# Kernel optimization log

Hardware: AMD Instinct MI355X
Metric: run time of the kernel (lower is better)

The kernel has to match this reference:

```python
import jax, jax.numpy as jnp
import numpy as np

LN_EPS = 1e-5
N, D = 512, 512


def setup_inputs() -> dict:
    key = jax.random.key(0)
    ks = jax.random.split(key, 3)
    s1 = 1.0 / np.sqrt(2 * D)  # torch Linear default-ish scale
    s2 = 1.0 / np.sqrt(D)
    return {
        "embeddings": jax.random.normal(ks[0], (N, D), jnp.float32),
        "W1": jax.random.normal(ks[1], (2 * D, D), jnp.float32) * s1,  # [in, out]
        "b1": jnp.zeros((D,), jnp.float32),
        "gamma": jnp.ones((D,), jnp.float32),
        "beta": jnp.zeros((D,), jnp.float32),
        "W2": jax.random.normal(ks[2], (D, 1), jnp.float32) * s2,
        "b2": jnp.zeros((1,), jnp.float32),
    }


def reference(embeddings, W1, b1, gamma, beta, W2, b2):
    d = embeddings.shape[-1]
    # Linear(2D -> D) on cat(e_i, e_j) decomposes into two GEMMs + broadcast add,
    # avoiding materializing the [N, N, 2D] concatenated pair tensor.
    left = embeddings @ W1[:d]              # [N, D]  (contribution of e_i)
    right = embeddings @ W1[d:] + b1        # [N, D]  (contribution of e_j + bias)
    h = left[:, None, :] + right[None, :, :]  # [N, N, D]
    # LayerNorm over last dim (eps matches torch default)
    mu = h.mean(axis=-1, keepdims=True)
    var = ((h - mu) ** 2).mean(axis=-1, keepdims=True)
    h = (h - mu) * jax.lax.rsqrt(var + LN_EPS) * gamma + beta
    # exact GELU (torch nn.GELU default)
    h = jax.nn.gelu(h, approximate=False)
    s = jax.nn.sigmoid(jnp.squeeze(h @ W2, -1) + b2[0])  # [N, N]
    # original loop only evaluates pairs i <= j and mirrors to (j, i)
    n = s.shape[0]
    upper = jnp.arange(n)[:, None] <= jnp.arange(n)[None, :]
    return jnp.where(upper, s, s.T)
```

## Files before the change

kernel.cpp:

```cpp
#include <hip/hip_runtime.h>


#define N_ 512
#define D_ 512

__global__ __launch_bounds__(256) void k_gemm(const float* __restrict__ E,
                                              const float* __restrict__ W1,
                                              const float* __restrict__ b1,
                                              float* __restrict__ W ) {
    __shared__ float e[16][516];
    const int t = threadIdx.x;
    const int cc = (blockIdx.x & 7) * 128;
    const int r0 = (blockIdx.x >> 3) * 16;
    const int half = cc >> 9;
    const int c = (cc & 511) + (t & 31) * 4;
    const int rp = (t >> 5) * 2;

    for (int x = t; x < 16 * 128; x += 256) {
        int r = x >> 7, c4 = (x & 127) << 2;
        *(float4*)&e[r][c4] = *(const float4*)&E[(r0 + r) * D_ + c4];
    }
    __syncthreads();

    const float* __restrict__ wp = W1 + (half << 18) + c;
    float4 a0 = {0.f, 0.f, 0.f, 0.f}, a1 = {0.f, 0.f, 0.f, 0.f};
#pragma unroll 4
    for (int k = 0; k < D_; k += 4) {
        float4 e0 = *(float4*)&e[rp][k];
        float4 e1 = *(float4*)&e[rp + 1][k];
        float4 wa = *(const float4*)(wp + ((k + 0) << 9));
        float4 wb = *(const float4*)(wp + ((k + 1) << 9));
        float4 wc = *(const float4*)(wp + ((k + 2) << 9));
        float4 wd = *(const float4*)(wp + ((k + 3) << 9));
        a0.x = fmaf(e0.x, wa.x, a0.x); a0.y = fmaf(e0.x, wa.y, a0.y);
        a0.z = fmaf(e0.x, wa.z, a0.z); a0.w = fmaf(e0.x, wa.w, a0.w);
        a1.x = fmaf(e1.x, wa.x, a1.x); a1.y = fmaf(e1.x, wa.y, a1.y);
        a1.z = fmaf(e1.x, wa.z, a1.z); a1.w = fmaf(e1.x, wa.w, a1.w);
        a0.x = fmaf(e0.y, wb.x, a0.x); a0.y = fmaf(e0.y, wb.y, a0.y);
        a0.z = fmaf(e0.y, wb.z, a0.z); a0.w = fmaf(e0.y, wb.w, a0.w);
        a1.x = fmaf(e1.y, wb.x, a1.x); a1.y = fmaf(e1.y, wb.y, a1.y);
        a1.z = fmaf(e1.y, wb.z, a1.z); a1.w = fmaf(e1.y, wb.w, a1.w);
        a0.x = fmaf(e0.z, wc.x, a0.x); a0.y = fmaf(e0.z, wc.y, a0.y);
        a0.z = fmaf(e0.z, wc.z, a0.z); a0.w = fmaf(e0.z, wc.w, a0.w);
        a1.x = fmaf(e1.z, wc.x, a1.x); a1.y = fmaf(e1.z, wc.y, a1.y);
        a1.z = fmaf(e1.z, wc.z, a1.z); a1.w = fmaf(e1.z, wc.w, a1.w);
        a0.x = fmaf(e0.w, wd.x, a0.x); a0.y = fmaf(e0.w, wd.y, a0.y);
        a0.z = fmaf(e0.w, wd.z, a0.z); a0.w = fmaf(e0.w, wd.w, a0.w);
        a1.x = fmaf(e1.w, wd.x, a1.x); a1.y = fmaf(e1.w, wd.y, a1.y);
        a1.z = fmaf(e1.w, wd.z, a1.z); a1.w = fmaf(e1.w, wd.w, a1.w);
    }
    if (half) {
        float4 bb = *(const float4*)(b1 + c);
        a0.x += bb.x; a0.y += bb.y; a0.z += bb.z; a0.w += bb.w;
        a1.x += bb.x; a1.y += bb.y; a1.z += bb.z; a1.w += bb.w;
    }
    *(float4*)(W + ((half << 9) + r0 + rp) * D_ + c) = a0;
    *(float4*)(W + ((half << 9) + r0 + rp + 1) * D_ + c) = a1;
}

__device__ __forceinline__ float block_sum(float v, float* sred, int t) {
#pragma unroll
    for (int off = 32; off > 0; off >>= 1) v += __shfl_xor(v, off, 64);
    int wave = t >> 6;
    if ((t & 63) == 0) sred[wave] = v;
    __syncthreads();
    float s = sred[0] + sred[1] + sred[2] + sred[3];
    __syncthreads();
    return s;
}

__global__ __launch_bounds__(256) void k_center(float* __restrict__ W,
                                                float* __restrict__ var) {
    __shared__ float sred[4];
    const int r = blockIdx.x, t = threadIdx.x;
    float* p = W + r * D_;
    float v0 = p[t], v1 = p[t + 256];
    float s = block_sum(v0 + v1, sred, t);
    float mean = s * (1.f / D_);
    float c0 = v0 - mean, c1 = v1 - mean;
    float ss = block_sum(c0 * c0 + c1 * c1, sred, t);
    p[t] = c0;
    p[t + 256] = c1;
    if (t == 0) var[r] = ss * (1.f / D_);
}

__device__ __forceinline__ void gelu_acc(float l, float r, float g, float be,
                                         float w, float rstd, float& acc) {
    float s = l + r;
    float x = fmaf(s * rstd, g, be);
    float x2 = x * x;
    float q = x * fmaf(-0.10294340f, x2, -2.30220935f);
    float eq = __builtin_amdgcn_exp2f(q);
    float ge = x * __builtin_amdgcn_rcpf(1.f + eq);
    acc = fmaf(ge, w, acc);
}

__global__ __launch_bounds__(256) void k_pair(const float* __restrict__ W,
                                              const float* __restrict__ var,
                                              const float* __restrict__ gf,
                                              const float* __restrict__ bef,
                                              const float* __restrict__ wf,
                                              const float* __restrict__ b2f,
                                              float* __restrict__ out) {
    __shared__ float ls[16][260];
    __shared__ float rs[16][260];
    __shared__ float red[4096];
    __shared__ float rstd_s[256];

    const int b = blockIdx.x;
    int I = (int)((65.0f - sqrtf(4225.0f - 8.0f * (float)b)) * 0.5f);
    if (I < 0) I = 0;
    if (I > 31) I = 31;
#define S_(i) (32 * (i) - ((i) * ((i)-1)) / 2)
    while (S_(I) > b) --I;
    while (S_(I + 1) <= b) ++I;
    const int J = I + (b - S_(I));
#undef S_

    const int t = threadIdx.x;
    const int ks = t & 15, pt = t >> 4;
    const int i4 = (pt & 3) * 4, j4 = (pt >> 2) * 4;
    const int Ibase = I * 16, Jbase = N_ + J * 16;

    float cv[16];
#pragma unroll
    for (int c = 0; c < 16; ++c) cv[c] = 0.f;
    for (int kb = 0; kb < D_; kb += 256) {
        for (int x = t; x < 16 * 64; x += 256) {
            int r = x >> 6, c4 = (x & 63) << 2;
            *(float4*)&ls[r][c4] = *(const float4*)&W[(Ibase + r) * D_ + kb + c4];
            *(float4*)&rs[r][c4] = *(const float4*)&W[(Jbase + r) * D_ + kb + c4];
        }
        __syncthreads();
#pragma unroll
        for (int it = 0; it < 4; ++it) {
            const int kq = (it * 16 + ks) * 4;
            float4 lq[4], rq[4];
#pragma unroll
            for (int d = 0; d < 4; ++d) {
                lq[d] = *(float4*)&ls[i4 + d][kq];
                rq[d] = *(float4*)&rs[j4 + d][kq];
            }
#pragma unroll
            for (int di = 0; di < 4; ++di)
#pragma unroll
                for (int dj = 0; dj < 4; ++dj)
                    cv[di * 4 + dj] += lq[di].x * rq[dj].x + lq[di].y * rq[dj].y +
                                       lq[di].z * rq[dj].z + lq[di].w * rq[dj].w;
        }
        __syncthreads();
    }
#pragma unroll
    for (int c = 0; c < 16; ++c) red[ks * 256 + pt * 16 + c] = cv[c];
    __syncthreads();

    const int ri = t >> 4, rj = t & 15;
    const int rpt = (ri >> 2) + ((rj >> 2) << 2);
    const int rc = (ri & 3) * 4 + (rj & 3);
    {
        float cov = 0.f;
#pragma unroll
        for (int k2 = 0; k2 < 16; ++k2) cov += red[k2 * 256 + rpt * 16 + rc];
        float varh = var[Ibase + ri] + var[Jbase + rj] + cov * (2.f / D_) + 1e-5f;
        rstd_s[t] = rsqrtf(varh);
    }
    __syncthreads();

    float rst[16];
#pragma unroll
    for (int di = 0; di < 4; ++di)
#pragma unroll
        for (int dj = 0; dj < 4; ++dj)
            rst[di * 4 + dj] = rstd_s[(i4 + di) * 16 + (j4 + dj)];
    float ac[16];
#pragma unroll
    for (int c = 0; c < 16; ++c) ac[c] = 0.f;
    for (int kb = 0; kb < D_; kb += 256) {
        for (int x = t; x < 16 * 64; x += 256) {
            int r = x >> 6, c4 = (x & 63) << 2;
            *(float4*)&ls[r][c4] = *(const float4*)&W[(Ibase + r) * D_ + kb + c4];
            *(float4*)&rs[r][c4] = *(const float4*)&W[(Jbase + r) * D_ + kb + c4];
        }
        __syncthreads();
#pragma unroll
        for (int it = 0; it < 4; ++it) {
            const int kq = (it * 16 + ks) * 4;
            float4 g4 = *(const float4*)&gf[kb + kq];
            float4 be4 = *(const float4*)&bef[kb + kq];
            float4 w4 = *(const float4*)&wf[kb + kq];
            float4 lq[4], rq[4];
#pragma unroll
            for (int d = 0; d < 4; ++d) {
                lq[d] = *(float4*)&ls[i4 + d][kq];
                rq[d] = *(float4*)&rs[j4 + d][kq];
            }
#pragma unroll
            for (int di = 0; di < 4; ++di)
#pragma unroll
                for (int dj = 0; dj < 4; ++dj) {
                    float rr = rst[di * 4 + dj];
                    float& a = ac[di * 4 + dj];
                    gelu_acc(lq[di].x, rq[dj].x, g4.x, be4.x, w4.x, rr, a);
                    gelu_acc(lq[di].y, rq[dj].y, g4.y, be4.y, w4.y, rr, a);
                    gelu_acc(lq[di].z, rq[dj].z, g4.z, be4.z, w4.z, rr, a);
                    gelu_acc(lq[di].w, rq[dj].w, g4.w, be4.w, w4.w, rr, a);
                }
        }
        __syncthreads();
    }
#pragma unroll
    for (int c = 0; c < 16; ++c) red[ks * 256 + pt * 16 + c] = ac[c];
    __syncthreads();

    {
        float z = b2f[0];
#pragma unroll
        for (int k2 = 0; k2 < 16; ++k2) z += red[k2 * 256 + rpt * 16 + rc];
        float sg = __builtin_amdgcn_rcpf(1.f + __builtin_amdgcn_exp2f(-1.44269504f * z));
        const int gi = Ibase + ri, gj = (Jbase - N_) + rj;
        if (gi <= gj) {
            out[gi * N_ + gj] = sg;
            out[gj * N_ + gi] = sg;
        }
    }
}

extern "C" void kernel_launch(void* const* d_in, const int* in_sizes, int n_in,
                              void* d_out, int out_size, void* d_ws, size_t ws_size,
                              hipStream_t stream) {
    const float* E     = (const float*)d_in[0];
    const float* W1    = (const float*)d_in[1];
    const float* b1    = (const float*)d_in[2];
    const float* gamma = (const float*)d_in[3];
    const float* beta  = (const float*)d_in[4];
    const float* w2    = (const float*)d_in[5];
    const float* b2    = (const float*)d_in[6];
    float* out = (float*)d_out;

    float* F    = (float*)d_ws;
    float* lcrc = F;
    float* var  = F + 1024 * 512;

    k_gemm<<<256, 256, 0, stream>>>(E, W1, b1, lcrc);
    k_center<<<1024, 256, 0, stream>>>(lcrc, var);
    k_pair<<<528, 256, 0, stream>>>(lcrc, var, gamma, beta, w2, b2, out);
}
```

Baseline: 132.0 us.

## Shrink pair-kernel shared memory for occupancy and split GEMM into smaller tiles

The pair kernel now stages W in 128-column chunks with padded rows and aliases the reduction buffer onto the staging area, cutting shared memory from about 50KB to about 17KB. It also adds a min-blocks hint of 4 to launch_bounds so more blocks can be resident per CU. The k-slice mapping is rearranged so each wave owns separate k-slices, and the reduction layout is transposed with padding to avoid bank conflicts. The GEMM kernel uses 64-column tiles with one row per thread and launches twice as many blocks, which halves register accumulators but re-reads weights more often.

After: 171.3 us. 29.8% more time.

```diff
diff --git a/kernel.cpp b/kernel.cpp
--- a/kernel.cpp
+++ b/kernel.cpp
@@ -8,54 +8,43 @@
                                               const float* __restrict__ W1,
                                               const float* __restrict__ b1,
                                               float* __restrict__ W ) {
-    __shared__ float e[16][516];
+    __shared__ float e[16 * 516];
     const int t = threadIdx.x;
-    const int cc = (blockIdx.x & 7) * 128;
-    const int r0 = (blockIdx.x >> 3) * 16;
+    const int cc = (blockIdx.x & 15) * 64;
+    const int r0 = (blockIdx.x >> 4) * 16;
     const int half = cc >> 9;
-    const int c = (cc & 511) + (t & 31) * 4;
-    const int rp = (t >> 5) * 2;
+    const int c = (cc & 511) + (t & 15) * 4;
+    const int r = t >> 4;
 
     for (int x = t; x < 16 * 128; x += 256) {
-        int r = x >> 7, c4 = (x & 127) << 2;
-        *(float4*)&e[r][c4] = *(const float4*)&E[(r0 + r) * D_ + c4];
+        int rr = x >> 7, q = x & 127;
+        *(float4*)&e[rr * 516 + q * 4] = *(const float4*)&E[(r0 + rr) * D_ + q * 4];
     }
     __syncthreads();
 
     const float* __restrict__ wp = W1 + (half << 18) + c;
-    float4 a0 = {0.f, 0.f, 0.f, 0.f}, a1 = {0.f, 0.f, 0.f, 0.f};
+    float4 acc = {0.f, 0.f, 0.f, 0.f};
 #pragma unroll 4
     for (int k = 0; k < D_; k += 4) {
-        float4 e0 = *(float4*)&e[rp][k];
-        float4 e1 = *(float4*)&e[rp + 1][k];
+        float4 e4 = *(float4*)&e[r * 516 + k];
         float4 wa = *(const float4*)(wp + ((k + 0) << 9));
         float4 wb = *(const float4*)(wp + ((k + 1) << 9));
         float4 wc = *(const float4*)(wp + ((k + 2) << 9));
         float4 wd = *(const float4*)(wp + ((k + 3) << 9));
-        a0.x = fmaf(e0.x, wa.x, a0.x); a0.y = fmaf(e0.x, wa.y, a0.y);
-        a0.z = fmaf(e0.x, wa.z, a0.z); a0.w = fmaf(e0.x, wa.w, a0.w);
-        a1.x = fmaf(e1.x, wa.x, a1.x); a1.y = fmaf(e1.x, wa.y, a1.y);
-        a1.z = fmaf(e1.x, wa.z, a1.z); a1.w = fmaf(e1.x, wa.w, a1.w);
-        a0.x = fmaf(e0.y, wb.x, a0.x); a0.y = fmaf(e0.y, wb.y, a0.y);
-        a0.z = fmaf(e0.y, wb.z, a0.z); a0.w = fmaf(e0.y, wb.w, a0.w);
-        a1.x = fmaf(e1.y, wb.x, a1.x); a1.y = fmaf(e1.y, wb.y, a1.y);
-        a1.z = fmaf(e1.y, wb.z, a1.z); a1.w = fmaf(e1.y, wb.w, a1.w);
-        a0.x = fmaf(e0.z, wc.x, a0.x); a0.y = fmaf(e0.z, wc.y, a0.y);
-        a0.z = fmaf(e0.z, wc.z, a0.z); a0.w = fmaf(e0.z, wc.w, a0.w);
-        a1.x = fmaf(e1.z, wc.x, a1.x); a1.y = fmaf(e1.z, wc.y, a1.y);
-        a1.z = fmaf(e1.z, wc.z, a1.z); a1.w = fmaf(e1.z, wc.w, a1.w);
-        a0.x = fmaf(e0.w, wd.x, a0.x); a0.y = fmaf(e0.w, wd.y, a0.y);
-        a0.z = fmaf(e0.w, wd.z, a0.z); a0.w = fmaf(e0.w, wd.w, a0.w);
-        a1.x = fmaf(e1.w, wd.x, a1.x); a1.y = fmaf(e1.w, wd.y, a1.y);
-        a1.z = fmaf(e1.w, wd.z, a1.z); a1.w = fmaf(e1.w, wd.w, a1.w);
+        acc.x = fmaf(e4.x, wa.x, acc.x); acc.y = fmaf(e4.x, wa.y, acc.y);
+        acc.z = fmaf(e4.x, wa.z, acc.z); acc.w = fmaf(e4.x, wa.w, acc.w);
+        acc.x = fmaf(e4.y, wb.x, acc.x); acc.y = fmaf(e4.y, wb.y, acc.y);
+        acc.z = fmaf(e4.y, wb.z, acc.z); acc.w = fmaf(e4.y, wb.w, acc.w);
+        acc.x = fmaf(e4.z, wc.x, acc.x); acc.y = fmaf(e4.z, wc.y, acc.y);
+        acc.z = fmaf(e4.z, wc.z, acc.z); acc.w = fmaf(e4.z, wc.w, acc.w);
+        acc.x = fmaf(e4.w, wd.x, acc.x); acc.y = fmaf(e4.w, wd.y, acc.y);
+        acc.z = fmaf(e4.w, wd.z, acc.z); acc.w = fmaf(e4.w, wd.w, acc.w);
     }
     if (half) {
         float4 bb = *(const float4*)(b1 + c);
-        a0.x += bb.x; a0.y += bb.y; a0.z += bb.z; a0.w += bb.w;
-        a1.x += bb.x; a1.y += bb.y; a1.z += bb.z; a1.w += bb.w;
-    }
-    *(float4*)(W + ((half << 9) + r0 + rp) * D_ + c) = a0;
-    *(float4*)(W + ((half << 9) + r0 + rp + 1) * D_ + c) = a1;
+        acc.x += bb.x; acc.y += bb.y; acc.z += bb.z; acc.w += bb.w;
+    }
+    *(float4*)(W + ((half << 9) + r0 + r) * D_ + c) = acc;
 }
 
 __device__ __forceinline__ float block_sum(float v, float* sred, int t) {
@@ -95,17 +84,18 @@
     acc = fmaf(ge, w, acc);
 }
 
-__global__ __launch_bounds__(256) void k_pair(const float* __restrict__ W,
-                                              const float* __restrict__ var,
-                                              const float* __restrict__ gf,
-                                              const float* __restrict__ bef,
-                                              const float* __restrict__ wf,
-                                              const float* __restrict__ b2f,
-                                              float* __restrict__ out) {
-    __shared__ float ls[16][260];
-    __shared__ float rs[16][260];
-    __shared__ float red[4096];
-    __shared__ float rstd_s[256];
+__global__ __launch_bounds__(256, 4) void k_pair(const float* __restrict__ W,
+                                                 const float* __restrict__ var,
+                                                 const float* __restrict__ gf,
+                                                 const float* __restrict__ bef,
+                                                 const float* __restrict__ wf,
+                                                 const float* __restrict__ b2f,
+                                                 float* __restrict__ out) {
+    __shared__ float smem[4416];
+    float* ls = smem;
+    float* rs = smem + 2080;
+    float* red = smem;
+    float* rstd_s = smem + 4160;
 
     const int b = blockIdx.x;
     int I = (int)((65.0f - sqrtf(4225.0f - 8.0f * (float)b)) * 0.5f);
@@ -118,28 +108,33 @@
 #undef S_
 
     const int t = threadIdx.x;
-    const int ks = t & 15, pt = t >> 4;
-    const int i4 = (pt & 3) * 4, j4 = (pt >> 2) * 4;
+    const int l = t & 63, wv = t >> 6;
+    const int pt = l & 15, s = l >> 4;
+    const int pi = pt & 3, pj = pt >> 2;
+    const int sigma = wv * 4 + s;
+    const int i4 = pi * 4, j4 = pj * 4;
     const int Ibase = I * 16, Jbase = N_ + J * 16;
 
     float cv[16];
 #pragma unroll
     for (int c = 0; c < 16; ++c) cv[c] = 0.f;
-    for (int kb = 0; kb < D_; kb += 256) {
-        for (int x = t; x < 16 * 64; x += 256) {
-            int r = x >> 6, c4 = (x & 63) << 2;
-            *(float4*)&ls[r][c4] = *(const float4*)&W[(Ibase + r) * D_ + kb + c4];
-            *(float4*)&rs[r][c4] = *(const float4*)&W[(Jbase + r) * D_ + kb + c4];
-        }
-        __syncthreads();
-#pragma unroll
-        for (int it = 0; it < 4; ++it) {
-            const int kq = (it * 16 + ks) * 4;
+    for (int c = 0; c < 4; ++c) {
+#pragma unroll
+        for (int it = 0; it < 2; ++it) {
+            int x = t + it * 256;
+            int rr = x >> 5, q = x & 31;
+            *(float4*)&ls[rr * 130 + q * 4] = *(const float4*)&W[(Ibase + rr) * D_ + c * 128 + q * 4];
+            *(float4*)&rs[rr * 130 + q * 4] = *(const float4*)&W[(Jbase + rr) * D_ + c * 128 + q * 4];
+        }
+        __syncthreads();
+#pragma unroll
+        for (int mm = 0; mm < 2; ++mm) {
+            const int off = 64 * mm + 4 * sigma;
             float4 lq[4], rq[4];
 #pragma unroll
             for (int d = 0; d < 4; ++d) {
-                lq[d] = *(float4*)&ls[i4 + d][kq];
-                rq[d] = *(float4*)&rs[j4 + d][kq];
+                lq[d] = *(float4*)&ls[(i4 + d) * 130 + off];
+                rq[d] = *(float4*)&rs[(j4 + d) * 130 + off];
             }
 #pragma unroll
             for (int di = 0; di < 4; ++di)
@@ -151,17 +146,18 @@
         __syncthreads();
     }
 #pragma unroll
-    for (int c = 0; c < 16; ++c) red[ks * 256 + pt * 16 + c] = cv[c];
-    __syncthreads();
-
-    const int ri = t >> 4, rj = t & 15;
-    const int rpt = (ri >> 2) + ((rj >> 2) << 2);
-    const int rc = (ri & 3) * 4 + (rj & 3);
+    for (int di = 0; di < 4; ++di)
+#pragma unroll
+        for (int dj = 0; dj < 4; ++dj)
+            red[sigma * 257 + (j4 + dj) * 16 + i4 + di] = cv[di * 4 + dj];
+    __syncthreads();
+
     {
-        float cov = 0.f;
-#pragma unroll
-        for (int k2 = 0; k2 < 16; ++k2) cov += red[k2 * 256 + rpt * 16 + rc];
-        float varh = var[Ibase + ri] + var[Jbase + rj] + cov * (2.f / D_) + 1e-5f;
+        const int ii = t & 15, jj = t >> 4;
+        float covsum = 0.f;
+#pragma unroll
+        for (int ss = 0; ss < 16; ++ss) covsum += red[ss * 257 + t];
+        float varh = var[Ibase + ii] + var[Jbase + jj] + covsum * (2.f / D_) + 1e-5f;
         rstd_s[t] = rsqrtf(varh);
     }
     __syncthreads();
@@ -171,53 +167,60 @@
     for (int di = 0; di < 4; ++di)
 #pragma unroll
         for (int dj = 0; dj < 4; ++dj)
-            rst[di * 4 + dj] = rstd_s[(i4 + di) * 16 + (j4 + dj)];
+            rst[di * 4 + dj] = rstd_s[(j4 + dj) * 16 + i4 + di];
     float ac[16];
 #pragma unroll
     for (int c = 0; c < 16; ++c) ac[c] = 0.f;
-    for (int kb = 0; kb < D_; kb += 256) {
-        for (int x = t; x < 16 * 64; x += 256) {
-            int r = x >> 6, c4 = (x & 63) << 2;
-            *(float4*)&ls[r][c4] = *(const float4*)&W[(Ibase + r) * D_ + kb + c4];
-            *(float4*)&rs[r][c4] = *(const float4*)&W[(Jbase + r) * D_ + kb + c4];
-        }
-        __syncthreads();
-#pragma unroll
-        for (int it = 0; it < 4; ++it) {
-            const int kq = (it * 16 + ks) * 4;
-            float4 g4 = *(const float4*)&gf[kb + kq];
-            float4 be4 = *(const float4*)&bef[kb + kq];
-            float4 w4 = *(const float4*)&wf[kb + kq];
+    for (int c = 0; c < 4; ++c) {
+#pragma unroll
+        for (int it = 0; it < 2; ++it) {
+            int x = t + it * 256;
+            int rr = x >> 5, q = x & 31;
+            *(float4*)&ls[rr * 130 + q * 4] = *(const float4*)&W[(Ibase + rr) * D_ + c * 128 + q * 4];
+            *(float4*)&rs[rr * 130 + q * 4] = *(const float4*)&W[(Jbase + rr) * D_ + c * 128 + q * 4];
+        }
+        __syncthreads();
+#pragma unroll
+        for (int mm = 0; mm < 2; ++mm) {
+            const int off = 64 * mm + 4 * sigma;
+            const int kg = c * 128 + off;
+            float4 g4 = *(const float4*)&gf[kg];
+            float4 be4 = *(const float4*)&bef[kg];
+            float4 w4 = *(const float4*)&wf[kg];
             float4 lq[4], rq[4];
 #pragma unroll
             for (int d = 0; d < 4; ++d) {
-                lq[d] = *(float4*)&ls[i4 + d][kq];
-                rq[d] = *(float4*)&rs[j4 + d][kq];
+                lq[d] = *(float4*)&ls[(i4 + d) * 130 + off];
+                rq[d] = *(float4*)&rs[(j4 + d) * 130 + off];
             }
 #pragma unroll
             for (int di = 0; di < 4; ++di)
 #pragma unroll
                 for (int dj = 0; dj < 4; ++dj) {
-                    float rr = rst[di * 4 + dj];
+                    float rr2 = rst[di * 4 + dj];
                     float& a = ac[di * 4 + dj];
-                    gelu_acc(lq[di].x, rq[dj].x, g4.x, be4.x, w4.x, rr, a);
-                    gelu_acc(lq[di].y, rq[dj].y, g4.y, be4.y, w4.y, rr, a);
-                    gelu_acc(lq[di].z, rq[dj].z, g4.z, be4.z, w4.z, rr, a);
-                    gelu_acc(lq[di].w, rq[dj].w, g4.w, be4.w, w4.w, rr, a);
+                    gelu_acc(lq[di].x, rq[dj].x, g4.x, be4.x, w4.x, rr2, a);
+                    gelu_acc(lq[di].y, rq[dj].y, g4.y, be4.y, w4.y, rr2, a);
+                    gelu_acc(lq[di].z, rq[dj].z, g4.z, be4.z, w4.z, rr2, a);
+                    gelu_acc(lq[di].w, rq[dj].w, g4.w, be4.w, w4.w, rr2, a);
                 }
         }
         __syncthreads();
     }
 #pragma unroll
-    for (int c = 0; c < 16; ++c) red[ks * 256 + pt * 16 + c] = ac[c];
+    for (int di = 0; di < 4; ++di)
+#pragma unroll
+        for (int dj = 0; dj < 4; ++dj)
+            red[sigma * 257 + (j4 + dj) * 16 + i4 + di] = ac[di * 4 + dj];
     __syncthreads();
 
     {
+        const int ii = t & 15, jj = t >> 4;
         float z = b2f[0];
 #pragma unroll
-        for (int k2 = 0; k2 < 16; ++k2) z += red[k2 * 256 + rpt * 16 + rc];
+        for (int ss = 0; ss < 16; ++ss) z += red[ss * 257 + t];
         float sg = __builtin_amdgcn_rcpf(1.f + __builtin_amdgcn_exp2f(-1.44269504f * z));
-        const int gi = Ibase + ri, gj = (Jbase - N_) + rj;
+        const int gi = Ibase + ii, gj = J * 16 + jj;
         if (gi <= gj) {
             out[gi * N_ + gj] = sg;
             out[gj * N_ + gi] = sg;
@@ -241,7 +244,7 @@
     float* lcrc = F;
     float* var  = F + 1024 * 512;
 
-    k_gemm<<<256, 256, 0, stream>>>(E, W1, b1, lcrc);
+    k_gemm<<<512, 256, 0, stream>>>(E, W1, b1, lcrc);
     k_center<<<1024, 256, 0, stream>>>(lcrc, var);
     k_pair<<<528, 256, 0, stream>>>(lcrc, var, gamma, beta, w2, b2, out);
 }
```
